# Kernel optimization log

Hardware: AMD Instinct MI355X
Metric: run time of the kernel (lower is better)

Reference implementation:

```python
import jax, jax.numpy as jnp
import numpy as np

NSTEP = 5  # mean-field iterations (module default)


def setup_inputs() -> dict:
    key = jax.random.key(0)
    k1, k2 = jax.random.split(key)
    N = 4096  # number of 'person' constants
    return {
        "logits_smoke": jax.random.normal(k1, (N, 2), dtype=jnp.float32),
        "logits_friend": jax.random.normal(k2, (N, N, 2), dtype=jnp.float32),
        "weights": jnp.ones((1,), dtype=jnp.float32) * 5.0,  # rule weight param
    }


def _mp_step(base_s, base_f, cur_s, cur_f, weights):
    # q-values via softmax over labels
    qs = jax.nn.softmax(cur_s, axis=-1)   # [N, 2]
    qf = jax.nn.softmax(cur_f, axis=-1)   # [N, N, 2]
    # per-atom 'unsatisfied' factors: 1 - sum(q * vals)
    # neg atom (vals=[1,0]) -> q[...,1]; pos atom (vals=[0,1]) -> q[...,0]
    s1 = qs[:, 1]        # !smoke(a) factor
    s0 = qs[:, 0]        # smoke(b) factor
    f1 = qf[:, :, 1]     # !friend(a,b) factor
    w0 = weights[0]
    # message to smoke(a) (neg target -> label 0): einsum 'ab,b->a'
    m_s0 = (f1 @ s0) * w0                      # [N]
    # message to smoke(b) (pos target -> label 1): einsum 'a,ab->b'
    m_s1 = (s1 @ f1) * w0                      # [N]
    # message to friend(a,b) (neg target -> label 0): einsum 'a,b->ab'
    m_f0 = (s1[:, None] * s0[None, :]) * w0    # [N, N]
    msg_s = jnp.stack([m_s0, m_s1], axis=-1)                   # [N, 2]
    msg_f = jnp.stack([m_f0, jnp.zeros_like(m_f0)], axis=-1)   # [N, N, 2]
    return base_s + msg_s, base_f + msg_f


def reference(logits_smoke, logits_friend, weights):
    cur_s, cur_f = logits_smoke, logits_friend
    for _ in range(NSTEP):
        cur_s, cur_f = _mp_step(logits_smoke, logits_friend, cur_s, cur_f, weights)
    return cur_s, cur_f
```

## Files before the change

kernel.cpp:

```cpp
#include <hip/hip_runtime.h>
#include <hip/hip_fp16.h>

#define NN 4096
constexpr int TPB = 256;
constexpr int NSTRIP = 4;
constexpr int CPB = 1024;
constexpr int RPB = 16;
constexpr int NROWG = NN / RPB;
constexpr int NRSLOT = NSTRIP * (TPB / 64);
constexpr int NBLK = NSTRIP * NROWG;

typedef float    f32x4 __attribute__((ext_vector_type(4)));
typedef _Float16 f16x4 __attribute__((ext_vector_type(4)));

__device__ __forceinline__ float sigmoidf_(float x) {
    return 1.0f / (1.0f + __expf(-x));
}

template <int MODE>
__global__ __launch_bounds__(TPB) void pass_kernel(
    const float2* __restrict__ bs, const f32x4* __restrict__ bf,
    f16x4* __restrict__ df, f32x4* __restrict__ of,
    const float* __restrict__ s1c, const float* __restrict__ s1p,
    const float* __restrict__ wptr,
    float* __restrict__ rowpart, float* __restrict__ colpart,
    float* __restrict__ s1store) {
    const int t = threadIdx.x;
    const int bid = blockIdx.x;
    const int strip = bid & (NSTRIP - 1);
    const int rg = bid >> 2;
    const int j0 = strip * CPB + t * 4;
    const int i0 = rg * RPB;
    const float w = wptr[0];

    float s0cv[4], ws0p[4];
#pragma unroll
    for (int k = 0; k < 4; ++k) {
        if (MODE <= 1) {
            float2 v = bs[j0 + k];
            s0cv[k] = 1.0f - sigmoidf_(v.y - v.x);
            ws0p[k] = 0.0f;
        } else {
            s0cv[k] = 1.0f - s1c[j0 + k];
            ws0p[k] = w * (1.0f - s1p[j0 + k]);
        }
    }
    if (MODE <= 1) {
        if (bid < NN / TPB) {
            int x = bid * TPB + t;
            float2 v = bs[x];
            s1store[x] = sigmoidf_(v.y - v.x);
        }
    }
    float colacc[4] = {0.f, 0.f, 0.f, 0.f};
    for (int r = 0; r < RPB; ++r) {
        const int i = i0 + r;
        float s1ci, s1pi;
        if (MODE <= 1) {
            float2 v = bs[i];
            s1ci = sigmoidf_(v.y - v.x);
            s1pi = 0.0f;
        } else {
            s1ci = s1c[i];
            s1pi = s1p[i];
        }
        float dd[4];
        if (MODE == 2) {
            f16x4 h = reinterpret_cast<const f16x4*>(df)[((size_t)i * NN + j0) >> 2];
            dd[0] = (float)h.x; dd[1] = (float)h.y;
            dd[2] = (float)h.z; dd[3] = (float)h.w;
        } else {
            const size_t u = ((size_t)i * NN + j0) >> 1;
            f32x4 a = bf[u];
            f32x4 b = bf[u + 1];
            dd[0] = a.y - a.x; dd[1] = a.w - a.z;
            dd[2] = b.y - b.x; dd[3] = b.w - b.z;
            if (MODE == 0) {
                f16x4 h;
                h.x = (_Float16)dd[0]; h.y = (_Float16)dd[1];
                h.z = (_Float16)dd[2]; h.w = (_Float16)dd[3];
                df[((size_t)i * NN + j0) >> 2] = h;
            }
            if (MODE == 4) {
                const float wi = w * s1ci;
                f32x4 oa = {a.x + wi * s0cv[0], a.y, a.z + wi * s0cv[1], a.w};
                f32x4 ob = {b.x + wi * s0cv[2], b.y, b.z + wi * s0cv[3], b.w};
                __builtin_nontemporal_store(oa, of + u);
                __builtin_nontemporal_store(ob, of + u + 1);
            }
        }
        float rowp = 0.f;
#pragma unroll
        for (int k = 0; k < 4; ++k) {
            float f1 = sigmoidf_(dd[k] - s1pi * ws0p[k]);
            colacc[k] += s1ci * f1;
            rowp += f1 * s0cv[k];
        }
#pragma unroll
        for (int off = 32; off > 0; off >>= 1) rowp += __shfl_down(rowp, off);
        if ((t & 63) == 0)
            rowpart[(size_t)(strip * (TPB / 64) + (t >> 6)) * NN + i] = rowp;
    }
    *reinterpret_cast<f32x4*>(colpart + (size_t)rg * NN + j0) =
        f32x4{colacc[0], colacc[1], colacc[2], colacc[3]};
}

__global__ __launch_bounds__(1024) void update_kernel(
    const float* __restrict__ rowpart, const float* __restrict__ colpart,
    const float2* __restrict__ bs, const float* __restrict__ wptr,
    float* __restrict__ s1next, float2* __restrict__ out_s, int writeOut) {
    __shared__ float red0[16][64];
    __shared__ float red1[16][64];
    const int col = threadIdx.x & 63;
    const int sl = threadIdx.x >> 6;
    const int x = blockIdx.x * 64 + col;

    float acc = 0.f;
    const int g0 = sl * (NROWG / 16);
#pragma unroll
    for (int g = g0; g < g0 + NROWG / 16; ++g) acc += colpart[(size_t)g * NN + x];
    red1[sl][col] = acc;
    red0[sl][col] = rowpart[(size_t)sl * NN + x];
    __syncthreads();
    if (sl == 0) {
        float m0 = 0.f, m1 = 0.f;
#pragma unroll
        for (int s = 0; s < 16; ++s) {
            m0 += red0[s][col];
            m1 += red1[s][col];
        }
        float w = wptr[0];
        float2 b = bs[x];
        float c0 = b.x + w * m0;
        float c1 = b.y + w * m1;
        if (writeOut) out_s[x] = make_float2(c0, c1);
        else s1next[x] = sigmoidf_(c1 - c0);
    }
}

extern "C" void kernel_launch(void* const* d_in, const int* in_sizes, int n_in,
                              void* d_out, int out_size, void* d_ws,
                              size_t ws_size, hipStream_t stream) {
    const float2* bs = (const float2*)d_in[0];
    const f32x4* bf = (const f32x4*)d_in[1];
    const float* wptr = (const float*)d_in[2];
    float2* out_s = (float2*)d_out;
    f32x4* out_f = (f32x4*)((float*)d_out + 2 * NN);

    char* ws = (char*)d_ws;
    size_t off = 0;
    auto alloc = [&](size_t bytes) {
        void* p = ws + off;
        off = (off + bytes + 255) & ~(size_t)255;
        return p;
    };
    float* sa = (float*)alloc((size_t)NN * 4);
    float* sb = (float*)alloc((size_t)NN * 4);
    float* sc = (float*)alloc((size_t)NN * 4);
    float* rowpart = (float*)alloc((size_t)NRSLOT * NN * 4);
    float* colpart = (float*)alloc((size_t)NROWG * NN * 4);
    f16x4* df = (f16x4*)(ws + off);
    const bool use_df = (ws_size >= off + (size_t)NN * NN * 2);

    const dim3 gP(NBLK), bP(TPB);
    const dim3 gU(NN / 64), bU(1024);

    if (use_df)
        pass_kernel<0><<<gP, bP, 0, stream>>>(bs, bf, df, nullptr, nullptr,
                                              nullptr, wptr, rowpart, colpart, sa);
    else
        pass_kernel<1><<<gP, bP, 0, stream>>>(bs, bf, df, nullptr, nullptr,
                                              nullptr, wptr, rowpart, colpart, sa);
    update_kernel<<<gU, bU, 0, stream>>>(rowpart, colpart, bs, wptr, sb, nullptr, 0);

    if (use_df) {
        pass_kernel<2><<<gP, bP, 0, stream>>>(bs, bf, df, nullptr, sb, sa, wptr,
                                              rowpart, colpart, nullptr);
        update_kernel<<<gU, bU, 0, stream>>>(rowpart, colpart, bs, wptr, sc, nullptr, 0);
        pass_kernel<2><<<gP, bP, 0, stream>>>(bs, bf, df, nullptr, sc, sb, wptr,
                                              rowpart, colpart, nullptr);
        update_kernel<<<gU, bU, 0, stream>>>(rowpart, colpart, bs, wptr, sa, nullptr, 0);
        pass_kernel<2><<<gP, bP, 0, stream>>>(bs, bf, df, nullptr, sa, sc, wptr,
                                              rowpart, colpart, nullptr);
        update_kernel<<<gU, bU, 0, stream>>>(rowpart, colpart, bs, wptr, sb, nullptr, 0);
    } else {
        pass_kernel<3><<<gP, bP, 0, stream>>>(bs, bf, df, nullptr, sb, sa, wptr,
                                              rowpart, colpart, nullptr);
        update_kernel<<<gU, bU, 0, stream>>>(rowpart, colpart, bs, wptr, sc, nullptr, 0);
        pass_kernel<3><<<gP, bP, 0, stream>>>(bs, bf, df, nullptr, sc, sb, wptr,
                                              rowpart, colpart, nullptr);
        update_kernel<<<gU, bU, 0, stream>>>(rowpart, colpart, bs, wptr, sa, nullptr, 0);
        pass_kernel<3><<<gP, bP, 0, stream>>>(bs, bf, df, nullptr, sa, sc, wptr,
                                              rowpart, colpart, nullptr);
        update_kernel<<<gU, bU, 0, stream>>>(rowpart, colpart, bs, wptr, sb, nullptr, 0);
    }
    pass_kernel<4><<<gP, bP, 0, stream>>>(bs, bf, df, out_f, sb, sa, wptr,
                                          rowpart, colpart, nullptr);
    update_kernel<<<gU, bU, 0, stream>>>(rowpart, colpart, bs, wptr, nullptr, out_s, 1);
}
```

Baseline: 151.5 us.

## Fuse update reduction into pass kernel via last-blocks atomic counter

Removes the separate update_kernel launches. Each pass block increments an atomic counter when it finishes, and the last 64 blocks spin until all blocks are done, then each reduces one 64-column slice of the row and column partials. This cuts five kernel launches and their launch gaps. The trade-offs are a memset per call, spin-waiting blocks, and correctness that depends on the final blocks not starving the others of residency.

After: 432.5 us. 186% more time.

```diff
diff --git a/kernel.cpp b/kernel.cpp
--- a/kernel.cpp
+++ b/kernel.cpp
@@ -9,12 +9,43 @@
 constexpr int NROWG = NN / RPB;
 constexpr int NRSLOT = NSTRIP * (TPB / 64);
 constexpr int NBLK = NSTRIP * NROWG;
+constexpr int NSLICE = 64;
 
 typedef float    f32x4 __attribute__((ext_vector_type(4)));
 typedef _Float16 f16x4 __attribute__((ext_vector_type(4)));
 
 __device__ __forceinline__ float sigmoidf_(float x) {
     return 1.0f / (1.0f + __expf(-x));
+}
+
+__device__ __forceinline__ void update_slice(
+    int slice, int t, const float* __restrict__ rowpart,
+    const float* __restrict__ colpart, const float2* __restrict__ bs, float w,
+    float* __restrict__ s1next, float2* __restrict__ out_s, int writeOut) {
+    __shared__ float red0[4][64];
+    __shared__ float red1[4][64];
+    const int col = t & 63;
+    const int q = t >> 6;
+    const int x = slice * 64 + col;
+
+    float acc1 = 0.f;
+#pragma unroll 8
+    for (int g = q * 64; g < q * 64 + 64; ++g) acc1 += colpart[(size_t)g * NN + x];
+    float acc0 = 0.f;
+#pragma unroll
+    for (int s = q * 4; s < q * 4 + 4; ++s) acc0 += rowpart[(size_t)s * NN + x];
+    red1[q][col] = acc1;
+    red0[q][col] = acc0;
+    __syncthreads();
+    if (q == 0) {
+        float m0 = red0[0][col] + red0[1][col] + red0[2][col] + red0[3][col];
+        float m1 = red1[0][col] + red1[1][col] + red1[2][col] + red1[3][col];
+        float2 b = bs[x];
+        float c0 = b.x + w * m0;
+        float c1 = b.y + w * m1;
+        if (writeOut) out_s[x] = make_float2(c0, c1);
+        else s1next[x] = sigmoidf_(c1 - c0);
+    }
 }
 
 template <int MODE>
@@ -24,7 +55,8 @@
     const float* __restrict__ s1c, const float* __restrict__ s1p,
     const float* __restrict__ wptr,
     float* __restrict__ rowpart, float* __restrict__ colpart,
-    float* __restrict__ s1store) {
+    float* __restrict__ s1store, unsigned* __restrict__ ctr,
+    float* __restrict__ s1next, float2* __restrict__ out_s, int writeOut) {
     const int t = threadIdx.x;
     const int bid = blockIdx.x;
     const int strip = bid & (NSTRIP - 1);
@@ -103,38 +135,25 @@
     }
     *reinterpret_cast<f32x4*>(colpart + (size_t)rg * NN + j0) =
         f32x4{colacc[0], colacc[1], colacc[2], colacc[3]};
-}
-
-__global__ __launch_bounds__(1024) void update_kernel(
-    const float* __restrict__ rowpart, const float* __restrict__ colpart,
-    const float2* __restrict__ bs, const float* __restrict__ wptr,
-    float* __restrict__ s1next, float2* __restrict__ out_s, int writeOut) {
-    __shared__ float red0[16][64];
-    __shared__ float red1[16][64];
-    const int col = threadIdx.x & 63;
-    const int sl = threadIdx.x >> 6;
-    const int x = blockIdx.x * 64 + col;
-
-    float acc = 0.f;
-    const int g0 = sl * (NROWG / 16);
-#pragma unroll
-    for (int g = g0; g < g0 + NROWG / 16; ++g) acc += colpart[(size_t)g * NN + x];
-    red1[sl][col] = acc;
-    red0[sl][col] = rowpart[(size_t)sl * NN + x];
+
+    __shared__ unsigned s_rank;
     __syncthreads();
-    if (sl == 0) {
-        float m0 = 0.f, m1 = 0.f;
-#pragma unroll
-        for (int s = 0; s < 16; ++s) {
-            m0 += red0[s][col];
-            m1 += red1[s][col];
-        }
-        float w = wptr[0];
-        float2 b = bs[x];
-        float c0 = b.x + w * m0;
-        float c1 = b.y + w * m1;
-        if (writeOut) out_s[x] = make_float2(c0, c1);
-        else s1next[x] = sigmoidf_(c1 - c0);
+    if (t == 0) {
+        __threadfence();
+        s_rank = atomicAdd(ctr, 1u);
+    }
+    __syncthreads();
+    const unsigned rank = s_rank;
+    if (rank >= (unsigned)(NBLK - NSLICE)) {
+        if (t == 0) {
+            while (__hip_atomic_load(ctr, __ATOMIC_ACQUIRE,
+                                     __HIP_MEMORY_SCOPE_AGENT) < (unsigned)NBLK)
+                __builtin_amdgcn_s_sleep(8);
+        }
+        __syncthreads();
+        __threadfence();
+        update_slice((int)(rank - (NBLK - NSLICE)), t, rowpart, colpart, bs, w,
+                     s1next, out_s, writeOut);
     }
 }
 
@@ -154,6 +173,7 @@
         off = (off + bytes + 255) & ~(size_t)255;
         return p;
     };
+    unsigned* ctrs = (unsigned*)alloc(8 * sizeof(unsigned));
     float* sa = (float*)alloc((size_t)NN * 4);
     float* sb = (float*)alloc((size_t)NN * 4);
     float* sc = (float*)alloc((size_t)NN * 4);
@@ -162,39 +182,41 @@
     f16x4* df = (f16x4*)(ws + off);
     const bool use_df = (ws_size >= off + (size_t)NN * NN * 2);
 
+    hipMemsetAsync(ctrs, 0, 8 * sizeof(unsigned), stream);
+
     const dim3 gP(NBLK), bP(TPB);
-    const dim3 gU(NN / 64), bU(1024);
-
-    if (use_df)
-        pass_kernel<0><<<gP, bP, 0, stream>>>(bs, bf, df, nullptr, nullptr,
-                                              nullptr, wptr, rowpart, colpart, sa);
-    else
-        pass_kernel<1><<<gP, bP, 0, stream>>>(bs, bf, df, nullptr, nullptr,
-                                              nullptr, wptr, rowpart, colpart, sa);
-    update_kernel<<<gU, bU, 0, stream>>>(rowpart, colpart, bs, wptr, sb, nullptr, 0);
 
     if (use_df) {
+        pass_kernel<0><<<gP, bP, 0, stream>>>(bs, bf, df, nullptr, nullptr, nullptr,
+                                              wptr, rowpart, colpart, sa, ctrs + 0,
+                                              sb, nullptr, 0);
         pass_kernel<2><<<gP, bP, 0, stream>>>(bs, bf, df, nullptr, sb, sa, wptr,
-                                              rowpart, colpart, nullptr);
-        update_kernel<<<gU, bU, 0, stream>>>(rowpart, colpart, bs, wptr, sc, nullptr, 0);
+                                              rowpart, colpart, nullptr, ctrs + 1,
+                                              sc, nullptr, 0);
         pass_kernel<2><<<gP, bP, 0, stream>>>(bs, bf, df, nullptr, sc, sb, wptr,
-                                              rowpart, colpart, nullptr);
-        update_kernel<<<gU, bU, 0, stream>>>(rowpart, colpart, bs, wptr, sa, nullptr, 0);
+                                              rowpart, colpart, nullptr, ctrs + 2,
+                                              sa, nullptr, 0);
         pass_kernel<2><<<gP, bP, 0, stream>>>(bs, bf, df, nullptr, sa, sc, wptr,
-                                              rowpart, colpart, nullptr);
-        update_kernel<<<gU, bU, 0, stream>>>(rowpart, colpart, bs, wptr, sb, nullptr, 0);
+                                              rowpart, colpart, nullptr, ctrs + 3,
+                                              sb, nullptr, 0);
+        pass_kernel<4><<<gP, bP, 0, stream>>>(bs, bf, df, out_f, sb, sa, wptr,
+                                              rowpart, colpart, nullptr, ctrs + 4,
+                                              nullptr, out_s, 1);
     } else {
+        pass_kernel<1><<<gP, bP, 0, stream>>>(bs, bf, df, nullptr, nullptr, nullptr,
+                                              wptr, rowpart, colpart, sa, ctrs + 0,
+                                              sb, nullptr, 0);
         pass_kernel<3><<<gP, bP, 0, stream>>>(bs, bf, df, nullptr, sb, sa, wptr,
-                                              rowpart, colpart, nullptr);
-        update_kernel<<<gU, bU, 0, stream>>>(rowpart, colpart, bs, wptr, sc, nullptr, 0);
+                                              rowpart, colpart, nullptr, ctrs + 1,
+                                              sc, nullptr, 0);
         pass_kernel<3><<<gP, bP, 0, stream>>>(bs, bf, df, nullptr, sc, sb, wptr,
-                                              rowpart, colpart, nullptr);
-        update_kernel<<<gU, bU, 0, stream>>>(rowpart, colpart, bs, wptr, sa, nullptr, 0);
+                                              rowpart, colpart, nullptr, ctrs + 2,
+                                              sa, nullptr, 0);
         pass_kernel<3><<<gP, bP, 0, stream>>>(bs, bf, df, nullptr, sa, sc, wptr,
-                                              rowpart, colpart, nullptr);
-        update_kernel<<<gU, bU, 0, stream>>>(rowpart, colpart, bs, wptr, sb, nullptr, 0);
-    }
-    pass_kernel<4><<<gP, bP, 0, stream>>>(bs, bf, df, out_f, sb, sa, wptr,
-                                          rowpart, colpart, nullptr);
-    update_kernel<<<gU, bU, 0, stream>>>(rowpart, colpart, bs, wptr, nullptr, out_s, 1);
-}
+                                              rowpart, colpart, nullptr, ctrs + 3,
+                                              sb, nullptr, 0);
+        pass_kernel<4><<<gP, bP, 0, stream>>>(bs, bf, df, out_f, sb, sa, wptr,
+                                              rowpart, colpart, nullptr, ctrs + 4,
+                                              nullptr, out_s, 1);
+    }
+}
```

## Replace partial-sum buffers and update kernels with fixed-point 64-bit atomics

Applied to the files above, without the earlier changes.

Removes the five separate update/reduction kernels by having each pass atomically accumulate row and column sums into 64-bit fixed-point integer buffers. The next pass recomputes the sigmoid values from those sums on the fly, and a tiny kernel produces the final smoke output. This cuts kernel launches and the partial-sum round trips through memory, and the integer accumulation keeps results deterministic. In exchange it adds a memset, global atomic contention (one atomic per wave per row plus four per thread for columns), and redundant sigmoid recomputation per block. The fixed-point format also cannot represent negative sums, which the positive sigmoid-product sums here never produce.

Result: slower. 250.2 us (+65.2%).

```diff
diff --git a/kernel.cpp b/kernel.cpp
--- a/kernel.cpp
+++ b/kernel.cpp
@@ -7,24 +7,48 @@
 constexpr int CPB = 1024;
 constexpr int RPB = 16;
 constexpr int NROWG = NN / RPB;
-constexpr int NRSLOT = NSTRIP * (TPB / 64);
 constexpr int NBLK = NSTRIP * NROWG;
 
 typedef float    f32x4 __attribute__((ext_vector_type(4)));
 typedef _Float16 f16x4 __attribute__((ext_vector_type(4)));
+typedef unsigned long long u64;
+
+constexpr double SCALE = 1099511627776.0;
+constexpr double INV_SCALE = 1.0 / 1099511627776.0;
 
 __device__ __forceinline__ float sigmoidf_(float x) {
     return 1.0f / (1.0f + __expf(-x));
 }
+__device__ __forceinline__ float fromI(u64 v) {
+    return (float)((double)v * INV_SCALE);
+}
 
-template <int MODE>
+template <int STEPK>
+__device__ __forceinline__ void sig_pair(
+    int idx, const float2* __restrict__ bs,
+    const u64* __restrict__ rsC, const u64* __restrict__ csC,
+    const u64* __restrict__ rsP, const u64* __restrict__ csP,
+    float w, float& sc, float& sp) {
+    float2 b = bs[idx];
+    if (STEPK == 1) { sc = sigmoidf_(b.y - b.x); sp = 0.f; return; }
+    float c0 = b.x + w * fromI(rsC[idx]);
+    float c1 = b.y + w * fromI(csC[idx]);
+    sc = sigmoidf_(c1 - c0);
+    if (STEPK == 2) {
+        sp = sigmoidf_(b.y - b.x);
+    } else {
+        sp = sigmoidf_((b.y + w * fromI(csP[idx])) - (b.x + w * fromI(rsP[idx])));
+    }
+}
+
+template <int STEPK, int SRC, int WRITE_DF, int EPI>
 __global__ __launch_bounds__(TPB) void pass_kernel(
     const float2* __restrict__ bs, const f32x4* __restrict__ bf,
     f16x4* __restrict__ df, f32x4* __restrict__ of,
-    const float* __restrict__ s1c, const float* __restrict__ s1p,
-    const float* __restrict__ wptr,
-    float* __restrict__ rowpart, float* __restrict__ colpart,
-    float* __restrict__ s1store) {
+    const u64* __restrict__ rsC, const u64* __restrict__ csC,
+    const u64* __restrict__ rsP, const u64* __restrict__ csP,
+    u64* __restrict__ rsO, u64* __restrict__ csO,
+    const float* __restrict__ wptr) {
     const int t = threadIdx.x;
     const int bid = blockIdx.x;
     const int strip = bid & (NSTRIP - 1);
@@ -36,55 +60,39 @@
     float s0cv[4], ws0p[4];
 #pragma unroll
     for (int k = 0; k < 4; ++k) {
-        if (MODE <= 1) {
-            float2 v = bs[j0 + k];
-            s0cv[k] = 1.0f - sigmoidf_(v.y - v.x);
-            ws0p[k] = 0.0f;
-        } else {
-            s0cv[k] = 1.0f - s1c[j0 + k];
-            ws0p[k] = w * (1.0f - s1p[j0 + k]);
-        }
-    }
-    if (MODE <= 1) {
-        if (bid < NN / TPB) {
-            int x = bid * TPB + t;
-            float2 v = bs[x];
-            s1store[x] = sigmoidf_(v.y - v.x);
-        }
+        float sc, sp;
+        sig_pair<STEPK>(j0 + k, bs, rsC, csC, rsP, csP, w, sc, sp);
+        s0cv[k] = 1.0f - sc;
+        ws0p[k] = w * (1.0f - sp);
     }
     float colacc[4] = {0.f, 0.f, 0.f, 0.f};
+
+#pragma unroll 4
     for (int r = 0; r < RPB; ++r) {
         const int i = i0 + r;
         float s1ci, s1pi;
-        if (MODE <= 1) {
-            float2 v = bs[i];
-            s1ci = sigmoidf_(v.y - v.x);
-            s1pi = 0.0f;
-        } else {
-            s1ci = s1c[i];
-            s1pi = s1p[i];
-        }
+        sig_pair<STEPK>(i, bs, rsC, csC, rsP, csP, w, s1ci, s1pi);
         float dd[4];
-        if (MODE == 2) {
-            f16x4 h = reinterpret_cast<const f16x4*>(df)[((size_t)i * NN + j0) >> 2];
+        if (SRC == 1) {
+            f16x4 h = df[((size_t)i * NN + j0) >> 2];
             dd[0] = (float)h.x; dd[1] = (float)h.y;
             dd[2] = (float)h.z; dd[3] = (float)h.w;
         } else {
             const size_t u = ((size_t)i * NN + j0) >> 1;
             f32x4 a = bf[u];
-            f32x4 b = bf[u + 1];
+            f32x4 b2 = bf[u + 1];
             dd[0] = a.y - a.x; dd[1] = a.w - a.z;
-            dd[2] = b.y - b.x; dd[3] = b.w - b.z;
-            if (MODE == 0) {
+            dd[2] = b2.y - b2.x; dd[3] = b2.w - b2.z;
+            if (WRITE_DF) {
                 f16x4 h;
                 h.x = (_Float16)dd[0]; h.y = (_Float16)dd[1];
                 h.z = (_Float16)dd[2]; h.w = (_Float16)dd[3];
                 df[((size_t)i * NN + j0) >> 2] = h;
             }
-            if (MODE == 4) {
+            if (EPI) {
                 const float wi = w * s1ci;
                 f32x4 oa = {a.x + wi * s0cv[0], a.y, a.z + wi * s0cv[1], a.w};
-                f32x4 ob = {b.x + wi * s0cv[2], b.y, b.z + wi * s0cv[3], b.w};
+                f32x4 ob = {b2.x + wi * s0cv[2], b2.y, b2.z + wi * s0cv[3], b2.w};
                 __builtin_nontemporal_store(oa, of + u);
                 __builtin_nontemporal_store(ob, of + u + 1);
             }
@@ -99,43 +107,21 @@
 #pragma unroll
         for (int off = 32; off > 0; off >>= 1) rowp += __shfl_down(rowp, off);
         if ((t & 63) == 0)
-            rowpart[(size_t)(strip * (TPB / 64) + (t >> 6)) * NN + i] = rowp;
+            atomicAdd(&rsO[i], (u64)((double)rowp * SCALE));
     }
-    *reinterpret_cast<f32x4*>(colpart + (size_t)rg * NN + j0) =
-        f32x4{colacc[0], colacc[1], colacc[2], colacc[3]};
+#pragma unroll
+    for (int k = 0; k < 4; ++k)
+        atomicAdd(&csO[j0 + k], (u64)((double)colacc[k] * SCALE));
 }
 
-__global__ __launch_bounds__(1024) void update_kernel(
-    const float* __restrict__ rowpart, const float* __restrict__ colpart,
-    const float2* __restrict__ bs, const float* __restrict__ wptr,
-    float* __restrict__ s1next, float2* __restrict__ out_s, int writeOut) {
-    __shared__ float red0[16][64];
-    __shared__ float red1[16][64];
-    const int col = threadIdx.x & 63;
-    const int sl = threadIdx.x >> 6;
-    const int x = blockIdx.x * 64 + col;
-
-    float acc = 0.f;
-    const int g0 = sl * (NROWG / 16);
-#pragma unroll
-    for (int g = g0; g < g0 + NROWG / 16; ++g) acc += colpart[(size_t)g * NN + x];
-    red1[sl][col] = acc;
-    red0[sl][col] = rowpart[(size_t)sl * NN + x];
-    __syncthreads();
-    if (sl == 0) {
-        float m0 = 0.f, m1 = 0.f;
-#pragma unroll
-        for (int s = 0; s < 16; ++s) {
-            m0 += red0[s][col];
-            m1 += red1[s][col];
-        }
-        float w = wptr[0];
-        float2 b = bs[x];
-        float c0 = b.x + w * m0;
-        float c1 = b.y + w * m1;
-        if (writeOut) out_s[x] = make_float2(c0, c1);
-        else s1next[x] = sigmoidf_(c1 - c0);
-    }
+__global__ __launch_bounds__(256) void outs_kernel(
+    const float2* __restrict__ bs, const u64* __restrict__ rs5,
+    const u64* __restrict__ cs5, const float* __restrict__ wptr,
+    float2* __restrict__ out_s) {
+    int x = blockIdx.x * 256 + threadIdx.x;
+    float w = wptr[0];
+    float2 b = bs[x];
+    out_s[x] = make_float2(b.x + w * fromI(rs5[x]), b.y + w * fromI(cs5[x]));
 }
 
 extern "C" void kernel_launch(void* const* d_in, const int* in_sizes, int n_in,
@@ -154,47 +140,40 @@
         off = (off + bytes + 255) & ~(size_t)255;
         return p;
     };
-    float* sa = (float*)alloc((size_t)NN * 4);
-    float* sb = (float*)alloc((size_t)NN * 4);
-    float* sc = (float*)alloc((size_t)NN * 4);
-    float* rowpart = (float*)alloc((size_t)NRSLOT * NN * 4);
-    float* colpart = (float*)alloc((size_t)NROWG * NN * 4);
+    u64* S = (u64*)alloc((size_t)5 * 2 * NN * sizeof(u64));
     f16x4* df = (f16x4*)(ws + off);
     const bool use_df = (ws_size >= off + (size_t)NN * NN * 2);
 
+    auto rs = [&](int k) { return S + (size_t)(k - 1) * 2 * NN; };
+    auto cs = [&](int k) { return S + (size_t)(k - 1) * 2 * NN + NN; };
+
+    hipMemsetAsync(S, 0, (size_t)5 * 2 * NN * sizeof(u64), stream);
+
     const dim3 gP(NBLK), bP(TPB);
-    const dim3 gU(NN / 64), bU(1024);
-
-    if (use_df)
-        pass_kernel<0><<<gP, bP, 0, stream>>>(bs, bf, df, nullptr, nullptr,
-                                              nullptr, wptr, rowpart, colpart, sa);
-    else
-        pass_kernel<1><<<gP, bP, 0, stream>>>(bs, bf, df, nullptr, nullptr,
-                                              nullptr, wptr, rowpart, colpart, sa);
-    update_kernel<<<gU, bU, 0, stream>>>(rowpart, colpart, bs, wptr, sb, nullptr, 0);
+    const u64* nil = nullptr;
 
     if (use_df) {
-        pass_kernel<2><<<gP, bP, 0, stream>>>(bs, bf, df, nullptr, sb, sa, wptr,
-                                              rowpart, colpart, nullptr);
-        update_kernel<<<gU, bU, 0, stream>>>(rowpart, colpart, bs, wptr, sc, nullptr, 0);
-        pass_kernel<2><<<gP, bP, 0, stream>>>(bs, bf, df, nullptr, sc, sb, wptr,
-                                              rowpart, colpart, nullptr);
-        update_kernel<<<gU, bU, 0, stream>>>(rowpart, colpart, bs, wptr, sa, nullptr, 0);
-        pass_kernel<2><<<gP, bP, 0, stream>>>(bs, bf, df, nullptr, sa, sc, wptr,
-                                              rowpart, colpart, nullptr);
-        update_kernel<<<gU, bU, 0, stream>>>(rowpart, colpart, bs, wptr, sb, nullptr, 0);
+        pass_kernel<1, 0, 1, 0><<<gP, bP, 0, stream>>>(
+            bs, bf, df, nullptr, nil, nil, nil, nil, rs(1), cs(1), wptr);
+        pass_kernel<2, 1, 0, 0><<<gP, bP, 0, stream>>>(
+            bs, bf, df, nullptr, rs(1), cs(1), nil, nil, rs(2), cs(2), wptr);
+        pass_kernel<3, 1, 0, 0><<<gP, bP, 0, stream>>>(
+            bs, bf, df, nullptr, rs(2), cs(2), rs(1), cs(1), rs(3), cs(3), wptr);
+        pass_kernel<3, 1, 0, 0><<<gP, bP, 0, stream>>>(
+            bs, bf, df, nullptr, rs(3), cs(3), rs(2), cs(2), rs(4), cs(4), wptr);
+        pass_kernel<3, 0, 0, 1><<<gP, bP, 0, stream>>>(
+            bs, bf, df, out_f, rs(4), cs(4), rs(3), cs(3), rs(5), cs(5), wptr);
     } else {
-        pass_kernel<3><<<gP, bP, 0, stream>>>(bs, bf, df, nullptr, sb, sa, wptr,
-                                              rowpart, colpart, nullptr);
-        update_kernel<<<gU, bU, 0, stream>>>(rowpart, colpart, bs, wptr, sc, nullptr, 0);
-        pass_kernel<3><<<gP, bP, 0, stream>>>(bs, bf, df, nullptr, sc, sb, wptr,
-                                              rowpart, colpart, nullptr);
-        update_kernel<<<gU, bU, 0, stream>>>(rowpart, colpart, bs, wptr, sa, nullptr, 0);
-        pass_kernel<3><<<gP, bP, 0, stream>>>(bs, bf, df, nullptr, sa, sc, wptr,
-                                              rowpart, colpart, nullptr);
-        update_kernel<<<gU, bU, 0, stream>>>(rowpart, colpart, bs, wptr, sb, nullptr, 0);
+        pass_kernel<1, 0, 0, 0><<<gP, bP, 0, stream>>>(
+            bs, bf, df, nullptr, nil, nil, nil, nil, rs(1), cs(1), wptr);
+        pass_kernel<2, 0, 0, 0><<<gP, bP, 0, stream>>>(
+            bs, bf, df, nullptr, rs(1), cs(1), nil, nil, rs(2), cs(2), wptr);
+        pass_kernel<3, 0, 0, 0><<<gP, bP, 0, stream>>>(
+            bs, bf, df, nullptr, rs(2), cs(2), rs(1), cs(1), rs(3), cs(3), wptr);
+        pass_kernel<3, 0, 0, 0><<<gP, bP, 0, stream>>>(
+            bs, bf, df, nullptr, rs(3), cs(3), rs(2), cs(2), rs(4), cs(4), wptr);
+        pass_kernel<3, 0, 0, 1><<<gP, bP, 0, stream>>>(
+            bs, bf, df, out_f, rs(4), cs(4), rs(3), cs(3), rs(5), cs(5), wptr);
     }
-    pass_kernel<4><<<gP, bP, 0, stream>>>(bs, bf, df, out_f, sb, sa, wptr,
-                                          rowpart, colpart, nullptr);
-    update_kernel<<<gU, bU, 0, stream>>>(rowpart, colpart, bs, wptr, nullptr, out_s, 1);
+    outs_kernel<<<NN / 256, 256, 0, stream>>>(bs, rs(5), cs(5), wptr, out_s);
 }
```
